# Performance work log

Measured on AMD Instinct MI355X. Metric: run time of the kernel, lower is better.

## Reference

```python
import jax, jax.numpy as jnp
import numpy as np

EPS = 1e-06
TEMP = 2.0

def _l2norm(x, eps=EPS):
    # F.normalize: x / max(||x||, eps)
    n = jnp.sqrt(jnp.sum(x * x, axis=-1, keepdims=True))
    return x / jnp.maximum(n, eps)

def setup_inputs() -> dict:
    key = jax.random.key(0)
    k1, k2 = jax.random.split(key)
    B, Lt, Lv, D = 8, 64, 16384, 256
    t = jax.random.normal(k1, (B, Lt, D), dtype=jnp.float32)
    v = jax.random.normal(k2, (B, Lv, D), dtype=jnp.float32)
    return {"t": t, "v": v}

def reference(t, v):
    dtype = v.dtype
    t = _l2norm(jnp.nan_to_num(t).astype(jnp.float32))
    v = _l2norm(jnp.nan_to_num(v).astype(jnp.float32))
    # S: [B, Lv, Lt]
    S = jnp.einsum('bvd,btd->bvt', v, t) / TEMP
    # text->vision attention: softmax over text axis (stable shift as in source)
    S_vt = jnp.nan_to_num(S - jnp.max(S, axis=2, keepdims=True))
    A_vt = jax.nn.softmax(S_vt, axis=2)            # [B, Lv, Lt]
    weights_vt = jax.nn.softmax(A_vt / TEMP, axis=1)  # softmax over vision axis
    text_score = jnp.sum(weights_vt * A_vt, axis=1)   # [B, Lt]
    text_score = text_score / (jnp.sum(text_score, axis=1, keepdims=True) + EPS)
    # vision<-text attention: per-sample loop in source == batched softmax over Lv
    S_tv = jnp.nan_to_num(S - jnp.max(S, axis=1, keepdims=True))
    A_tv = jax.nn.softmax(S_tv, axis=1)            # softmax over vision axis, [B, Lv, Lt]
    scores = jnp.einsum('bvt,bt->bv', A_tv, text_score)  # [B, Lv]
    mn = jnp.min(scores, axis=1, keepdims=True)
    mx = jnp.max(scores, axis=1, keepdims=True)
    scores = (scores - mn) / (mx - mn + EPS)
    return scores.astype(dtype)
```

## Files before the change

kernel.cpp:

```cpp
#include <hip/hip_runtime.h>
#include <stdint.h>

#define NB 8
#define LT 64
#define LV 16384
#define DD 256
#define EPSV 1e-6f
#define BF16MAX 3.3895313892515355e38f

typedef unsigned short u16t;
typedef __attribute__((ext_vector_type(8))) short short8;
typedef __attribute__((ext_vector_type(4))) float floatx4;

__device__ __forceinline__ float bf2f(u16t h) {
    union { uint32_t u; float f; } cv; cv.u = ((uint32_t)h) << 16; return cv.f;
}
__device__ __forceinline__ uint32_t asu(float f) { union { float f; uint32_t u; } c; c.f = f; return c.u; }
__device__ __forceinline__ float asf(uint32_t u) { union { uint32_t u; float f; } c; c.u = u; return c.f; }
__device__ __forceinline__ u16t f2bf(float f) {
    uint32_t u = asu(f);
    return (u16t)((u + 0x7fffu + ((u >> 16) & 1u)) >> 16);
}
__device__ __forceinline__ float fixnum(float f) {
    if (f != f) return 0.0f;
    if (f > BF16MAX) return BF16MAX;
    if (f < -BF16MAX) return -BF16MAX;
    return f;
}
__device__ __forceinline__ float load_in(const void* p, long i, int isf32) {
    return isf32 ? ((const float*)p)[i] : bf2f(((const u16t*)p)[i]);
}
__device__ __forceinline__ uint32_t bfhead(float a, float& hf) {
    uint32_t u = asu(a);
    uint32_t h = (u + 0x7fffu + ((u >> 16) & 1u)) >> 16;
    hf = asf(h << 16);
    return h;
}

__global__ void k_sniff(const u16t* v, int* flag) {
    int lane = threadIdx.x;
    int sane = 0;
    for (int i = 0; i < 16; ++i) {
        u16t h = v[lane * 16 + i];
        int ex = (h >> 7) & 0xFF;
        if ((h & 0x7FFF) == 0 || (ex >= 96 && ex < 160)) ++sane;
    }
    #pragma unroll
    for (int o = 1; o < 64; o <<= 1) sane += __shfl_xor(sane, o, 64);
    if (lane == 0) flag[0] = (sane < 900) ? 1 : 0;
}

__global__ void k0_zero(float* Z) {
    int i = blockIdx.x * 256 + threadIdx.x;
    if (i < 1536) Z[i] = 0.0f;
}

__global__ void k1_tnorm(const void* t, u16t* tnB, const int* flag) {
    __shared__ float red[256];
    int isf32 = flag[0];
    int row = blockIdx.x;
    int k = threadIdx.x;
    float x = fixnum(load_in(t, (long)row * DD + k, isf32));
    red[k] = x * x;
    __syncthreads();
    for (int s = 128; s > 0; s >>= 1) {
        if (k < s) red[k] += red[k + s];
        __syncthreads();
    }
    float scale = 0.5f / fmaxf(sqrtf(red[0]), EPSV);
    tnB[row * DD + k] = f2bf(x * scale);
}

__global__ __launch_bounds__(256) void k_gemm(const void* v, const u16t* tnB,
                                              float* Z, float* S1, float* S2,
                                              const float* c, float* scores,
                                              const int* flag, int mode) {
    __shared__ u16t ldsT[64 * 264];
    __shared__ float zlds[3][4][64];
    int isf32 = flag[0];
    int tid = threadIdx.x, wave = tid >> 6, lane = tid & 63;
    int c16 = lane & 15, q = lane >> 4;
    int b = blockIdx.y, tile = blockIdx.x;
    int rowbase = tile * 128 + wave * 32;

    {
        const u16t* src = tnB + (size_t)b * (LT * DD);
        for (int i = tid; i < 2048; i += 256) {
            int tt = i >> 5, k8 = i & 31;
            *(uint4*)&ldsT[tt * 264 + k8 * 8] = *(const uint4*)&src[tt * DD + k8 * 8];
        }
    }
    __syncthreads();

    floatx4 acc[2][4];
    #pragma unroll
    for (int mt = 0; mt < 2; ++mt)
        #pragma unroll
        for (int nt = 0; nt < 4; ++nt) acc[mt][nt] = (floatx4){0.f, 0.f, 0.f, 0.f};
    float ssqp[2] = {0.f, 0.f};

    for (int kc = 0; kc < 8; ++kc) {
        short8 bf[4];
        #pragma unroll
        for (int nt = 0; nt < 4; ++nt)
            bf[nt] = *(const short8*)&ldsT[(nt * 16 + c16) * 264 + kc * 32 + q * 8];

        #pragma unroll
        for (int mt = 0; mt < 2; ++mt) {
            int row = rowbase + mt * 16 + c16;
            float f[8];
            if (isf32) {
                const float* vr = (const float*)v +
                    ((size_t)b * LV + row) * DD + kc * 32 + q * 8;
                float4 p0 = *(const float4*)vr;
                float4 p1 = *(const float4*)(vr + 4);
                f[0]=p0.x; f[1]=p0.y; f[2]=p0.z; f[3]=p0.w;
                f[4]=p1.x; f[5]=p1.y; f[6]=p1.z; f[7]=p1.w;
            } else {
                const u16t* vr = (const u16t*)v +
                    ((size_t)b * LV + row) * DD + kc * 32 + q * 8;
                uint4 u = *(const uint4*)vr;
                f[0]=bf2f((u16t)u.x); f[1]=bf2f((u16t)(u.x>>16));
                f[2]=bf2f((u16t)u.y); f[3]=bf2f((u16t)(u.y>>16));
                f[4]=bf2f((u16t)u.z); f[5]=bf2f((u16t)(u.z>>16));
                f[6]=bf2f((u16t)u.w); f[7]=bf2f((u16t)(u.w>>16));
            }
            #pragma unroll
            for (int i = 0; i < 8; ++i) f[i] = fixnum(f[i]);
            union { short8 s; uint32_t u[4]; } a1, a2, a3;
            #pragma unroll
            for (int i = 0; i < 4; ++i) {
                float e0 = f[2*i], e1 = f[2*i+1];
                ssqp[mt] += e0 * e0 + e1 * e1;
                float h10f, h11f, h20f, h21f, dummy;
                uint32_t h10 = bfhead(e0, h10f), h11 = bfhead(e1, h11f);
                float r10 = e0 - h10f,  r11 = e1 - h11f;
                uint32_t h20 = bfhead(r10, h20f), h21 = bfhead(r11, h21f);
                float r20 = r10 - h20f, r21 = r11 - h21f;
                uint32_t h30 = bfhead(r20, dummy), h31 = bfhead(r21, dummy);
                a1.u[i] = h10 | (h11 << 16);
                a2.u[i] = h20 | (h21 << 16);
                a3.u[i] = h30 | (h31 << 16);
            }
            #pragma unroll
            for (int nt = 0; nt < 4; ++nt) {
                acc[mt][nt] = __builtin_amdgcn_mfma_f32_16x16x32_bf16(
                    a1.s, bf[nt], acc[mt][nt], 0, 0, 0);
                acc[mt][nt] = __builtin_amdgcn_mfma_f32_16x16x32_bf16(
                    a2.s, bf[nt], acc[mt][nt], 0, 0, 0);
                acc[mt][nt] = __builtin_amdgcn_mfma_f32_16x16x32_bf16(
                    a3.s, bf[nt], acc[mt][nt], 0, 0, 0);
            }
        }
    }

    float ssqf[2];
    #pragma unroll
    for (int mt = 0; mt < 2; ++mt) {
        float s = ssqp[mt];
        s += __shfl_xor(s, 16, 64);
        s += __shfl_xor(s, 32, 64);
        ssqf[mt] = s;
    }
    float facr[2][4];
    #pragma unroll
    for (int mt = 0; mt < 2; ++mt)
        #pragma unroll
        for (int reg = 0; reg < 4; ++reg) {
            float ss = __shfl(ssqf[mt], q * 4 + reg, 64);
            facr[mt][reg] = 1.0f / fmaxf(sqrtf(ss), EPSV);
        }

    if (mode == 0) {
        float zacc[4] = {0,0,0,0}, s1acc[4] = {0,0,0,0}, s2acc[4] = {0,0,0,0};
        #pragma unroll
        for (int mt = 0; mt < 2; ++mt)
            #pragma unroll
            for (int reg = 0; reg < 4; ++reg) {
                float e[4], se = 0.f;
                #pragma unroll
                for (int nt = 0; nt < 4; ++nt) {
                    e[nt] = __expf(acc[mt][nt][reg] * facr[mt][reg]);
                    se += e[nt];
                }
                se += __shfl_xor(se, 1, 64);
                se += __shfl_xor(se, 2, 64);
                se += __shfl_xor(se, 4, 64);
                se += __shfl_xor(se, 8, 64);
                float inv = 1.0f / se;
                #pragma unroll
                for (int nt = 0; nt < 4; ++nt) {
                    float A = e[nt] * inv;
                    float w = __expf(0.5f * A);
                    zacc[nt] += e[nt]; s1acc[nt] += w; s2acc[nt] += w * A;
                }
            }
        #pragma unroll
        for (int nt = 0; nt < 4; ++nt) {
            zacc[nt]  += __shfl_xor(zacc[nt], 16, 64);  zacc[nt]  += __shfl_xor(zacc[nt], 32, 64);
            s1acc[nt] += __shfl_xor(s1acc[nt], 16, 64); s1acc[nt] += __shfl_xor(s1acc[nt], 32, 64);
            s2acc[nt] += __shfl_xor(s2acc[nt], 16, 64); s2acc[nt] += __shfl_xor(s2acc[nt], 32, 64);
        }
        if (lane < 16) {
            #pragma unroll
            for (int nt = 0; nt < 4; ++nt) {
                zlds[0][wave][nt * 16 + lane] = zacc[nt];
                zlds[1][wave][nt * 16 + lane] = s1acc[nt];
                zlds[2][wave][nt * 16 + lane] = s2acc[nt];
            }
        }
        __syncthreads();
        if (tid < 64) {
            float z  = zlds[0][0][tid] + zlds[0][1][tid] + zlds[0][2][tid] + zlds[0][3][tid];
            float a  = zlds[1][0][tid] + zlds[1][1][tid] + zlds[1][2][tid] + zlds[1][3][tid];
            float s2 = zlds[2][0][tid] + zlds[2][1][tid] + zlds[2][2][tid] + zlds[2][3][tid];
            atomicAdd(&Z[b * LT + tid], z);
            atomicAdd(&S1[b * LT + tid], a);
            atomicAdd(&S2[b * LT + tid], s2);
        }
    } else {
        float cc[4];
        #pragma unroll
        for (int nt = 0; nt < 4; ++nt) cc[nt] = c[b * LT + nt * 16 + c16];
        #pragma unroll
        for (int mt = 0; mt < 2; ++mt)
            #pragma unroll
            for (int reg = 0; reg < 4; ++reg) {
                float x = 0.f;
                #pragma unroll
                for (int nt = 0; nt < 4; ++nt)
                    x += __expf(acc[mt][nt][reg] * facr[mt][reg]) * cc[nt];
                x += __shfl_xor(x, 1, 64);
                x += __shfl_xor(x, 2, 64);
                x += __shfl_xor(x, 4, 64);
                x += __shfl_xor(x, 8, 64);
                if (c16 == 0)
                    scores[(size_t)b * LV + rowbase + mt * 16 + q * 4 + reg] = x;
            }
    }
}

__global__ __launch_bounds__(64) void k3_coef(const float* Z, const float* S1,
                                              const float* S2, float* c) {
    int b = blockIdx.x, lane = threadIdx.x;
    float ts = S2[b * LT + lane] / S1[b * LT + lane];
    float tot = ts;
    #pragma unroll
    for (int o = 1; o < 64; o <<= 1) tot += __shfl_xor(tot, o, 64);
    c[b * LT + lane] = ts / ((tot + EPSV) * Z[b * LT + lane]);
}

__global__ __launch_bounds__(256) void k_mnmx(const float* scores, float* mnmx) {
    __shared__ float rmn[256], rmx[256];
    int b = blockIdx.x, tid = threadIdx.x;
    float mn = 3.4e38f, mx = -3.4e38f;
    for (int i = tid; i < LV; i += 256) {
        float x = scores[b * LV + i];
        mn = fminf(mn, x); mx = fmaxf(mx, x);
    }
    rmn[tid] = mn; rmx[tid] = mx;
    __syncthreads();
    for (int s = 128; s > 0; s >>= 1) {
        if (tid < s) {
            rmn[tid] = fminf(rmn[tid], rmn[tid + s]);
            rmx[tid] = fmaxf(rmx[tid], rmx[tid + s]);
        }
        __syncthreads();
    }
    if (tid == 0) { mnmx[b * 2] = rmn[0]; mnmx[b * 2 + 1] = rmx[0]; }
}

__global__ __launch_bounds__(256) void k5_out(const float* scores, const float* mnmx,
                                              void* out, const int* flag) {
    int isf32 = flag[0];
    int i = blockIdx.x * 256 + threadIdx.x;
    if (i >= NB * LV) return;
    int b = i >> 14;
    float mn = mnmx[b * 2], mx = mnmx[b * 2 + 1];
    float val = (scores[i] - mn) / (mx - mn + EPSV);
    if (isf32) ((float*)out)[i] = val;
    else ((u16t*)out)[i] = f2bf(val);
}

extern "C" void kernel_launch(void* const* d_in, const int* in_sizes, int n_in,
                              void* d_out, int out_size, void* d_ws, size_t ws_size,
                              hipStream_t stream) {
    const void* t = d_in[0];
    const void* v = d_in[1];
    char* w = (char*)d_ws;

    u16t*  tnB    = (u16t*)w;
    float* scores = (float*)(w + 262144);
    float* Z      = (float*)(w + 786432);
    float* S1     = Z + 512;
    float* S2     = Z + 1024;
    float* c      = Z + 1536;
    float* mnmx   = Z + 2048;
    int*   flag   = (int*)(Z + 2064);

    k_sniff<<<1, 64, 0, stream>>>((const u16t*)v, flag);
    k0_zero<<<6, 256, 0, stream>>>(Z);
    k1_tnorm<<<512, 256, 0, stream>>>(t, tnB, flag);
    k_gemm<<<dim3(128, NB), 256, 0, stream>>>(v, tnB, Z, S1, S2, nullptr, nullptr, flag, 0);
    k3_coef<<<NB, 64, 0, stream>>>(Z, S1, S2, c);
    k_gemm<<<dim3(128, NB), 256, 0, stream>>>(v, tnB, Z, S1, S2, c, scores, flag, 1);
    k_mnmx<<<NB, 256, 0, stream>>>(scores, mnmx);
    k5_out<<<512, 256, 0, stream>>>(scores, mnmx, d_out, flag);
}
```

Measured before the change: 266.6 us.

## Cache exp matrix from first GEMM pass and fuse score min/max reduction

The first GEMM pass now writes the unnormalized exponentials for every (row, text) pair to a workspace buffer. A new lightweight kernel computes scores as a dot product of those cached values with the per-text coefficients. This replaces the second full GEMM pass, which re-read v. The same kernel folds the per-batch min/max into block reductions plus unsigned atomics on float bits, which is valid because scores are non-negative. The cost is a 32 MB write and read of the cached matrix, and the path only runs when the workspace is large enough; otherwise the old path is kept.

```diff
diff --git a/kernel.cpp b/kernel.cpp
--- a/kernel.cpp
+++ b/kernel.cpp
@@ -53,6 +53,11 @@
 __global__ void k0_zero(float* Z) {
     int i = blockIdx.x * 256 + threadIdx.x;
     if (i < 1536) Z[i] = 0.0f;
+    else if (i < 1552) {
+        unsigned* u = (unsigned*)(Z + 2048);
+        int j = i - 1536;
+        u[j] = (j & 1) ? 0u : 0x7F7FFFFFu;
+    }
 }
 
 __global__ void k1_tnorm(const void* t, u16t* tnB, const int* flag) {
@@ -74,6 +79,7 @@
 __global__ __launch_bounds__(256) void k_gemm(const void* v, const u16t* tnB,
                                               float* Z, float* S1, float* S2,
                                               const float* c, float* scores,
+                                              float* E,
                                               const int* flag, int mode) {
     __shared__ u16t ldsT[64 * 264];
     __shared__ float zlds[3][4][64];
@@ -188,6 +194,12 @@
                 se += __shfl_xor(se, 4, 64);
                 se += __shfl_xor(se, 8, 64);
                 float inv = 1.0f / se;
+                if (E) {
+                    size_t rbase = ((((size_t)b << 14) + rowbase + mt * 16 + q * 4 + reg) << 6);
+                    #pragma unroll
+                    for (int nt = 0; nt < 4; ++nt)
+                        E[rbase + nt * 16 + c16] = e[nt];
+                }
                 #pragma unroll
                 for (int nt = 0; nt < 4; ++nt) {
                     float A = e[nt] * inv;
@@ -250,6 +262,55 @@
     c[b * LT + lane] = ts / ((tot + EPSV) * Z[b * LT + lane]);
 }
 
+__global__ __launch_bounds__(256) void k2_scores(const float* E, const float* c,
+                                                 float* scores, unsigned* mnmxU) {
+    __shared__ float cl[64];
+    __shared__ float rmn[256], rmx[256];
+    int tid = threadIdx.x;
+    int b = blockIdx.x >> 6;
+    if (tid < 64) cl[tid] = c[b * LT + tid];
+    __syncthreads();
+    size_t row = (size_t)blockIdx.x * 256 + tid;
+    const float* er = E + (row << 6);
+    float f[64];
+    #pragma unroll
+    for (int j = 0; j < 16; ++j) {
+        float4 v4 = *(const float4*)(er + j * 4);
+        f[j*4+0] = v4.x; f[j*4+1] = v4.y; f[j*4+2] = v4.z; f[j*4+3] = v4.w;
+    }
+    float p[16];
+    #pragma unroll
+    for (int i = 0; i < 16; ++i) {
+        float x = 0.f;
+        #pragma unroll
+        for (int nt = 0; nt < 4; ++nt) x += f[nt * 16 + i] * cl[nt * 16 + i];
+        p[i] = x;
+    }
+    float q1[8], q2[4], q3[2];
+    #pragma unroll
+    for (int j = 0; j < 8; ++j) q1[j] = p[2*j] + p[2*j+1];
+    #pragma unroll
+    for (int j = 0; j < 4; ++j) q2[j] = q1[2*j] + q1[2*j+1];
+    #pragma unroll
+    for (int j = 0; j < 2; ++j) q3[j] = q2[2*j] + q2[2*j+1];
+    float x = q3[0] + q3[1];
+    scores[row] = x;
+
+    rmn[tid] = x; rmx[tid] = x;
+    __syncthreads();
+    for (int s = 128; s > 0; s >>= 1) {
+        if (tid < s) {
+            rmn[tid] = fminf(rmn[tid], rmn[tid + s]);
+            rmx[tid] = fmaxf(rmx[tid], rmx[tid + s]);
+        }
+        __syncthreads();
+    }
+    if (tid == 0) {
+        atomicMin(&mnmxU[b * 2],     asu(rmn[0]));
+        atomicMax(&mnmxU[b * 2 + 1], asu(rmx[0]));
+    }
+}
+
 __global__ __launch_bounds__(256) void k_mnmx(const float* scores, float* mnmx) {
     __shared__ float rmn[256], rmx[256];
     int b = blockIdx.x, tid = threadIdx.x;
@@ -289,21 +350,47 @@
     const void* v = d_in[1];
     char* w = (char*)d_ws;
 
-    u16t*  tnB    = (u16t*)w;
-    float* scores = (float*)(w + 262144);
-    float* Z      = (float*)(w + 786432);
-    float* S1     = Z + 512;
-    float* S2     = Z + 1024;
-    float* c      = Z + 1536;
-    float* mnmx   = Z + 2048;
-    int*   flag   = (int*)(Z + 2064);
-
-    k_sniff<<<1, 64, 0, stream>>>((const u16t*)v, flag);
-    k0_zero<<<6, 256, 0, stream>>>(Z);
-    k1_tnorm<<<512, 256, 0, stream>>>(t, tnB, flag);
-    k_gemm<<<dim3(128, NB), 256, 0, stream>>>(v, tnB, Z, S1, S2, nullptr, nullptr, flag, 0);
-    k3_coef<<<NB, 64, 0, stream>>>(Z, S1, S2, c);
-    k_gemm<<<dim3(128, NB), 256, 0, stream>>>(v, tnB, Z, S1, S2, c, scores, flag, 1);
-    k_mnmx<<<NB, 256, 0, stream>>>(scores, mnmx);
-    k5_out<<<512, 256, 0, stream>>>(scores, mnmx, d_out, flag);
-}
+    const size_t E_BYTES = (size_t)NB * LV * LT * 4;
+    const size_t NEED_NEW = E_BYTES + 262144 + 524288 + 2080 * 4;
+
+    if (ws_size >= NEED_NEW) {
+        float* E      = (float*)w;
+        u16t*  tnB    = (u16t*)(w + E_BYTES);
+        float* scores = (float*)(w + E_BYTES + 262144);
+        float* Z      = (float*)(w + E_BYTES + 262144 + 524288);
+        float* S1     = Z + 512;
+        float* S2     = Z + 1024;
+        float* c      = Z + 1536;
+        unsigned* mnmxU = (unsigned*)(Z + 2048);
+        int*   flag   = (int*)(Z + 2064);
+
+        k_sniff<<<1, 64, 0, stream>>>((const u16t*)v, flag);
+        k0_zero<<<7, 256, 0, stream>>>(Z);
+        k1_tnorm<<<512, 256, 0, stream>>>(t, tnB, flag);
+        k_gemm<<<dim3(128, NB), 256, 0, stream>>>(v, tnB, Z, S1, S2, nullptr, nullptr,
+                                                  E, flag, 0);
+        k3_coef<<<NB, 64, 0, stream>>>(Z, S1, S2, c);
+        k2_scores<<<512, 256, 0, stream>>>(E, c, scores, mnmxU);
+        k5_out<<<512, 256, 0, stream>>>(scores, (const float*)mnmxU, d_out, flag);
+    } else {
+        u16t*  tnB    = (u16t*)w;
+        float* scores = (float*)(w + 262144);
+        float* Z      = (float*)(w + 786432);
+        float* S1     = Z + 512;
+        float* S2     = Z + 1024;
+        float* c      = Z + 1536;
+        float* mnmx   = Z + 2048;
+        int*   flag   = (int*)(Z + 2064);
+
+        k_sniff<<<1, 64, 0, stream>>>((const u16t*)v, flag);
+        k0_zero<<<6, 256, 0, stream>>>(Z);
+        k1_tnorm<<<512, 256, 0, stream>>>(t, tnB, flag);
+        k_gemm<<<dim3(128, NB), 256, 0, stream>>>(v, tnB, Z, S1, S2, nullptr, nullptr,
+                                                  nullptr, flag, 0);
+        k3_coef<<<NB, 64, 0, stream>>>(Z, S1, S2, c);
+        k_gemm<<<dim3(128, NB), 256, 0, stream>>>(v, tnB, Z, S1, S2, c, scores,
+                                                  nullptr, flag, 1);
+        k_mnmx<<<NB, 256, 0, stream>>>(scores, mnmx);
+        k5_out<<<512, 256, 0, stream>>>(scores, mnmx, d_out, flag);
+    }
+}
```

After: 236.7 us. 11.2% less time.
